# Optimization experiments

Measured on AMD Instinct MI355X. Metric: run time of the kernel, lower is better.

## Reference

```python
import jax, jax.numpy as jnp
import numpy as np

D_MODEL = 1024
NUM_HEADS = 16
HEAD_DIM = D_MODEL // NUM_HEADS


def setup_inputs() -> dict:
    key = jax.random.key(0)
    ks = jax.random.split(key, 6)
    B, S = 2, 2048
    w_scale = 1.0 / np.sqrt(D_MODEL)  # keep logits O(1) so the naive exp-softmax is stable
    return {
        "x": jax.random.normal(ks[0], (B, S, D_MODEL), dtype=jnp.float32),
        "y": jax.random.normal(ks[1], (B, S, D_MODEL), dtype=jnp.float32),
        "mask": jnp.zeros((S, S), dtype=jnp.float32),
        "Wq": jax.random.normal(ks[2], (D_MODEL, D_MODEL), dtype=jnp.float32) * w_scale,
        "Wk": jax.random.normal(ks[3], (D_MODEL, D_MODEL), dtype=jnp.float32) * w_scale,
        "Wv": jax.random.normal(ks[4], (D_MODEL, D_MODEL), dtype=jnp.float32) * w_scale,
        "Wo": jax.random.normal(ks[5], (D_MODEL, D_MODEL), dtype=jnp.float32) * w_scale,
    }


def _naive_softmax(s):
    # faithful to nirmalya_softmax: plain exp, sum + eps, no max subtraction
    p1 = jnp.exp(s)
    p2 = jnp.sum(p1, axis=-1, keepdims=True) + 1e-10
    return p1 / p2


def reference(x, y, mask, Wq, Wk, Wv, Wo):
    B, S, _ = x.shape
    # nn.Linear(bias=False): t @ W.T ; split heads -> [B, H, S, Dh]
    def split_heads(t):
        return t.reshape(B, S, NUM_HEADS, HEAD_DIM).transpose(0, 2, 1, 3)

    k = split_heads(x @ Wk.T)
    v = split_heads(x @ Wv.T)
    q = split_heads(y @ Wq.T)

    scores = jnp.einsum("bhqd,bhkd->bhqk", q, k) / np.sqrt(HEAD_DIM)
    scores = scores + mask  # [S,S] broadcasts over [B,H,S,S] (same math as permute-add-permute)
    attn = _naive_softmax(scores)
    out = jnp.einsum("bhqk,bhkd->bhqd", attn, v)  # [B,H,S,Dh]
    out = out.transpose(0, 2, 1, 3).reshape(B, S, D_MODEL)
    return out @ Wo.T
```

## Files before the change

kernel.cpp:

```cpp
#include <hip/hip_runtime.h>
#include <stdint.h>

typedef unsigned short u16;
typedef __attribute__((ext_vector_type(4))) float f32x4;
typedef __attribute__((ext_vector_type(2))) __bf16 bf16x2;
typedef __attribute__((ext_vector_type(8))) __bf16 bf16x8;
typedef __attribute__((ext_vector_type(4))) u16 u16x4;

#define AS1 __attribute__((address_space(1)))
#define AS3 __attribute__((address_space(3)))
#define GLOAD_LDS16(gp, lp) \
  __builtin_amdgcn_global_load_lds((const AS1 void*)(gp), (AS3 void*)(lp), 16, 0, 0)

__device__ __forceinline__ u16 f2bf(float f) {
  union { float f; unsigned u; } v; v.f = f;
  return (u16)((v.u + 0x7FFFu + ((v.u >> 16) & 1u)) >> 16);
}

__device__ __forceinline__ u16x4 pack4(float a, float b, float c, float d) {
#if __has_builtin(__builtin_amdgcn_cvt_pk_bf16_f32)
  union { struct { bf16x2 lo, hi; } p; u16x4 v; } u;
  u.p.lo = __builtin_amdgcn_cvt_pk_bf16_f32(a, b);
  u.p.hi = __builtin_amdgcn_cvt_pk_bf16_f32(c, d);
  return u.v;
#else
  u16x4 r; r.x = f2bf(a); r.y = f2bf(b); r.z = f2bf(c); r.w = f2bf(d); return r;
#endif
}

__global__ __launch_bounds__(256) void convert_all(
    const float* __restrict__ x, const float* __restrict__ y,
    const float* __restrict__ wq, const float* __restrict__ wk,
    const float* __restrict__ wv, const float* __restrict__ wo,
    u16* __restrict__ xb, u16* __restrict__ yb, u16* __restrict__ wqb,
    u16* __restrict__ wkb, u16* __restrict__ wvb, u16* __restrict__ wob) {
  size_t i = (size_t)blockIdx.x * 256 + threadIdx.x;
  const float* src; u16* dst; float scale = 1.0f; size_t off;
  if (i < (size_t)(1u << 20)) { src = x; dst = xb; off = i; }
  else if (i < (size_t)(2u << 20)) { src = y; dst = yb; off = i - (1u << 20); }
  else {
    size_t j = i - (size_t)(2u << 20);
    unsigned w = (unsigned)(j >> 18); off = j & ((1u << 18) - 1);
    if (w == 0)      { src = wq; dst = wqb; scale = 0.125f; }
    else if (w == 1) { src = wk; dst = wkb; }
    else if (w == 2) { src = wv; dst = wvb; }
    else             { src = wo; dst = wob; }
  }
  f32x4 v = ((const f32x4*)src)[off];
  ((u16x4*)dst)[off] = pack4(v.x * scale, v.y * scale, v.z * scale, v.w * scale);
}

__device__ __forceinline__ void gemm_core(
    const u16* __restrict__ A, const u16* __restrict__ Bt, int tm, int tn,
    u16* As, u16* Bs, f32x4 acc[4][4], int wave, int lane) {
  constexpr int K = 1024;
  const int l15 = lane & 15, quad = lane >> 4;
  const int wr = wave >> 1, wc = wave & 1;
  const int srow = lane >> 2;
  const int scol = ((lane & 3) ^ ((lane >> 3) & 3)) * 8;
  const u16* Ag = A + (size_t)(tm + wave * 32 + srow) * K + scol;
  const u16* Bg = Bt + (size_t)(tn + wave * 32 + srow) * K + scol;
  u16* Asl0 = &As[(wave * 2 + 0) * 512];
  u16* Asl1 = &As[(wave * 2 + 1) * 512];
  u16* Bsl0 = &Bs[(wave * 2 + 0) * 512];
  u16* Bsl1 = &Bs[(wave * 2 + 1) * 512];
  const int rc = (quad ^ ((l15 >> 1) & 3)) * 8;

  for (int k0 = 0; k0 < K; k0 += 32) {
    __syncthreads();
    GLOAD_LDS16(Ag + k0, Asl0);
    GLOAD_LDS16(Ag + 16 * K + k0, Asl1);
    GLOAD_LDS16(Bg + k0, Bsl0);
    GLOAD_LDS16(Bg + 16 * K + k0, Bsl1);
    __syncthreads();
    bf16x8 af[4], bfr[4];
#pragma unroll
    for (int mi = 0; mi < 4; ++mi)
      af[mi] = *(const bf16x8*)&As[(wr * 64 + mi * 16 + l15) * 32 + rc];
#pragma unroll
    for (int ni = 0; ni < 4; ++ni)
      bfr[ni] = *(const bf16x8*)&Bs[(wc * 64 + ni * 16 + l15) * 32 + rc];
#pragma unroll
    for (int mi = 0; mi < 4; ++mi)
#pragma unroll
      for (int ni = 0; ni < 4; ++ni)
        acc[mi][ni] = __builtin_amdgcn_mfma_f32_16x16x32_bf16(
            af[mi], bfr[ni], acc[mi][ni], 0, 0, 0);
  }
}

__global__ __launch_bounds__(256, 2) void qkv_gemm(
    const u16* __restrict__ xb, const u16* __restrict__ yb,
    const u16* __restrict__ wqb, const u16* __restrict__ wkb,
    const u16* __restrict__ wvb,
    u16* __restrict__ Qw, u16* __restrict__ Kw, u16* __restrict__ Vtw) {
  __shared__ __align__(16) u16 As[128 * 32];
  __shared__ __align__(16) u16 Bs[128 * 32];
  const int tid = threadIdx.x, wave = tid >> 6, lane = tid & 63;
  const int l15 = lane & 15, quad = lane >> 4;
  const int wr = wave >> 1, wc = wave & 1;
  const int z = blockIdx.z;
  const u16 *A, *Bt; int tm, tn;
  if (z == 0)      { A = yb;  Bt = wqb; tm = blockIdx.y * 128; tn = blockIdx.x * 128; }
  else if (z == 1) { A = xb;  Bt = wkb; tm = blockIdx.y * 128; tn = blockIdx.x * 128; }
  else             { A = wvb; Bt = xb;  tm = blockIdx.x * 128; tn = blockIdx.y * 128; }

  f32x4 acc[4][4] = {};
  gemm_core(A, Bt, tm, tn, As, Bs, acc, wave, lane);

#pragma unroll
  for (int mi = 0; mi < 4; ++mi) {
#pragma unroll
    for (int ni = 0; ni < 4; ++ni) {
#pragma unroll
      for (int r = 0; r < 4; ++r) {
        int gm = tm + wr * 64 + mi * 16 + quad * 4 + r;
        int gn = tn + wc * 64 + ni * 16 + l15;
        u16 val = f2bf(acc[mi][ni][r]);
        if (z == 2) {
          int h = gm >> 6, dh = gm & 63, b = gn >> 11, s = gn & 2047;
          Vtw[(((size_t)(b * 16 + h) * 64 + dh) << 11) + s] = val;
        } else {
          int b = gm >> 11, s = gm & 2047, h = gn >> 6, dh = gn & 63;
          u16* dst = (z == 0) ? Qw : Kw;
          dst[(((size_t)(b * 16 + h) * 2048 + s) << 6) + dh] = val;
        }
      }
    }
  }
}

__global__ __launch_bounds__(256, 2) void out_gemm(
    const u16* __restrict__ Ow, const u16* __restrict__ wob,
    float* __restrict__ C) {
  __shared__ __align__(16) u16 As[128 * 32];
  __shared__ __align__(16) u16 Bs[128 * 32];
  const int tid = threadIdx.x, wave = tid >> 6, lane = tid & 63;
  const int l15 = lane & 15, quad = lane >> 4;
  const int wr = wave >> 1, wc = wave & 1;
  const int tm = blockIdx.y * 128, tn = blockIdx.x * 128;

  f32x4 acc[4][4] = {};
  gemm_core(Ow, wob, tm, tn, As, Bs, acc, wave, lane);

#pragma unroll
  for (int mi = 0; mi < 4; ++mi)
#pragma unroll
    for (int ni = 0; ni < 4; ++ni)
#pragma unroll
      for (int r = 0; r < 4; ++r) {
        int gm = tm + wr * 64 + mi * 16 + quad * 4 + r;
        int gn = tn + wc * 64 + ni * 16 + l15;
        C[(size_t)gm * 1024 + gn] = acc[mi][ni][r];
      }
}

__global__ __launch_bounds__(256, 3) void attn_kernel(
    const u16* __restrict__ Qw, const u16* __restrict__ Kw,
    const u16* __restrict__ Vtw, const float* __restrict__ mask,
    u16* __restrict__ Ow) {
  constexpr int S = 2048;
  constexpr int PADK = 136;
  __shared__ __align__(16) u16 Ks[128 * 64];
  __shared__ __align__(16) u16 Vs[64 * 128];
  __shared__ __align__(16) u16 Ps[64 * PADK];
  const int tid = threadIdx.x;
  const int wave = tid >> 6, lane = tid & 63;
  const int l15 = lane & 15, quad = lane >> 4;
  const int qt = blockIdx.x, h = blockIdx.y, b = blockIdx.z;
  const size_t head = ((size_t)(b * 16 + h)) * S * 64;
  const int q_global = qt * 64 + wave * 16 + l15;

  bf16x8 qf[2];
#pragma unroll
  for (int kq = 0; kq < 2; ++kq)
    qf[kq] = *(const bf16x8*)&Qw[head + (size_t)q_global * 64 + kq * 32 + quad * 8];

  const __bf16 one_bf = (__bf16)1.0f;
  const bf16x8 ones = {one_bf, one_bf, one_bf, one_bf, one_bf, one_bf, one_bf, one_bf};

  f32x4 oa[4] = {};
  f32x4 den = {};

  const int k_r = lane >> 3;
  const int k_c = ((lane & 7) ^ ((lane >> 3) & 7)) * 8;
  const int v_r = lane >> 4;
  const int v_cbase = lane & 15;
  const float* mrow = mask + (size_t)q_global * S;

  for (int kt = 0; kt < S; kt += 128) {
    __syncthreads();
#pragma unroll
    for (int c = 0; c < 4; ++c) {
      int g = wave * 4 + c;
      GLOAD_LDS16(&Kw[head + (size_t)(kt + g * 8 + k_r) * 64 + k_c], &Ks[g * 512]);
    }
#pragma unroll
    for (int c = 0; c < 4; ++c) {
      int g = wave * 4 + c;
      int dh = g * 4 + v_r;
      int scb = (v_cbase ^ (dh & 15)) * 8;
      GLOAD_LDS16(&Vtw[head + (size_t)dh * S + kt + scb], &Vs[g * 512]);
    }
    f32x4 mv[8];
#pragma unroll
    for (int mk = 0; mk < 8; ++mk)
      mv[mk] = *(const f32x4*)&mrow[kt + mk * 16 + quad * 4];
    __syncthreads();

    f32x4 sa[8] = {};
#pragma unroll
    for (int kq = 0; kq < 2; ++kq) {
#pragma unroll
      for (int mk = 0; mk < 8; ++mk) {
        int row = mk * 16 + l15;
        bf16x8 ak = *(const bf16x8*)&Ks[row * 64 + (((kq * 4 + quad) ^ (l15 & 7)) * 8)];
        sa[mk] = __builtin_amdgcn_mfma_f32_16x16x32_bf16(ak, qf[kq], sa[mk], 0, 0, 0);
      }
    }

#pragma unroll
    for (int mk = 0; mk < 8; ++mk) {
      float p0 = __expf(sa[mk][0] + mv[mk][0]);
      float p1 = __expf(sa[mk][1] + mv[mk][1]);
      float p2 = __expf(sa[mk][2] + mv[mk][2]);
      float p3 = __expf(sa[mk][3] + mv[mk][3]);
      *(u16x4*)&Ps[(wave * 16 + l15) * PADK + mk * 16 + quad * 4] = pack4(p0, p1, p2, p3);
    }

#pragma unroll
    for (int kq2 = 0; kq2 < 4; ++kq2) {
      bf16x8 ap = *(const bf16x8*)&Ps[(wave * 16 + l15) * PADK + kq2 * 32 + quad * 8];
#pragma unroll
      for (int nv = 0; nv < 4; ++nv) {
        int row = nv * 16 + l15;
        bf16x8 bv = *(const bf16x8*)&Vs[row * 128 + (((kq2 * 4 + quad) ^ l15) * 8)];
        oa[nv] = __builtin_amdgcn_mfma_f32_16x16x32_bf16(ap, bv, oa[nv], 0, 0, 0);
      }
      den = __builtin_amdgcn_mfma_f32_16x16x32_bf16(ap, ones, den, 0, 0, 0);
    }
  }

#pragma unroll
  for (int nv = 0; nv < 4; ++nv) {
#pragma unroll
    for (int r = 0; r < 4; ++r) {
      int srow = qt * 64 + wave * 16 + quad * 4 + r;
      int dh = nv * 16 + l15;
      float val = oa[nv][r] / (den[r] + 1e-10f);
      Ow[((size_t)(b * S + srow) << 10) + h * 64 + dh] = f2bf(val);
    }
  }
}

extern "C" void kernel_launch(void* const* d_in, const int* in_sizes, int n_in,
                              void* d_out, int out_size, void* d_ws, size_t ws_size,
                              hipStream_t stream) {
  const float* x    = (const float*)d_in[0];
  const float* y    = (const float*)d_in[1];
  const float* mask = (const float*)d_in[2];
  const float* Wq   = (const float*)d_in[3];
  const float* Wk   = (const float*)d_in[4];
  const float* Wv   = (const float*)d_in[5];
  const float* Wo   = (const float*)d_in[6];
  char* ws = (char*)d_ws;
  const size_t MB = (size_t)1 << 20;
  u16* xb  = (u16*)(ws + 0  * MB);
  u16* yb  = (u16*)(ws + 8  * MB);
  u16* wqb = (u16*)(ws + 16 * MB);
  u16* wkb = (u16*)(ws + 18 * MB);
  u16* wvb = (u16*)(ws + 20 * MB);
  u16* wob = (u16*)(ws + 22 * MB);
  u16* Qw  = (u16*)(ws + 24 * MB);
  u16* Kw  = (u16*)(ws + 32 * MB);
  u16* Vtw = (u16*)(ws + 40 * MB);
  u16* Ow  = (u16*)(ws + 48 * MB);

  convert_all<<<12288, 256, 0, stream>>>(x, y, Wq, Wk, Wv, Wo,
                                         xb, yb, wqb, wkb, wvb, wob);
  qkv_gemm<<<dim3(8, 32, 3), 256, 0, stream>>>(xb, yb, wqb, wkb, wvb, Qw, Kw, Vtw);
  attn_kernel<<<dim3(32, 16, 2), 256, 0, stream>>>(Qw, Kw, Vtw, mask, Ow);
  out_gemm<<<dim3(8, 32), 256, 0, stream>>>(Ow, wob, (float*)d_out);
  (void)in_sizes; (void)n_in; (void)out_size; (void)ws_size;
}
```

Baseline: 267.5 us.

## Widen GEMM K-tile, double attention query rows, use exp2 and bf16 mask

The GEMM core now stages 64-wide K tiles with an 8-way XOR swizzle, which halves the number of barrier-separated iterations. The attention kernel gives each wave 32 query rows so every K/V fragment loaded from LDS feeds two MFMAs. Softmax switches to exp2, with log2e folded into Wq and the mask. The mask is converted to bf16 and stored temporarily in the output buffer, halving mask traffic, at the cost of rounding the mask and an extra conversion pass.

```diff
diff --git a/kernel.cpp b/kernel.cpp
--- a/kernel.cpp
+++ b/kernel.cpp
@@ -16,7 +16,16 @@
   union { float f; unsigned u; } v; v.f = f;
   return (u16)((v.u + 0x7FFFu + ((v.u >> 16) & 1u)) >> 16);
 }
-
+__device__ __forceinline__ float bf2f(u16 u) {
+  union { unsigned u; float f; } v; v.u = ((unsigned)u) << 16; return v.f;
+}
+__device__ __forceinline__ float fexp2(float x) {
+#if __has_builtin(__builtin_amdgcn_exp2f)
+  return __builtin_amdgcn_exp2f(x);
+#else
+  return exp2f(x);
+#endif
+}
 __device__ __forceinline__ u16x4 pack4(float a, float b, float c, float d) {
 #if __has_builtin(__builtin_amdgcn_cvt_pk_bf16_f32)
   union { struct { bf16x2 lo, hi; } p; u16x4 v; } u;
@@ -28,74 +37,81 @@
 #endif
 }
 
+#define LOG2E 1.44269504f
+
 __global__ __launch_bounds__(256) void convert_all(
     const float* __restrict__ x, const float* __restrict__ y,
     const float* __restrict__ wq, const float* __restrict__ wk,
     const float* __restrict__ wv, const float* __restrict__ wo,
+    const float* __restrict__ mask,
     u16* __restrict__ xb, u16* __restrict__ yb, u16* __restrict__ wqb,
-    u16* __restrict__ wkb, u16* __restrict__ wvb, u16* __restrict__ wob) {
+    u16* __restrict__ wkb, u16* __restrict__ wvb, u16* __restrict__ wob,
+    u16* __restrict__ maskb) {
   size_t i = (size_t)blockIdx.x * 256 + threadIdx.x;
   const float* src; u16* dst; float scale = 1.0f; size_t off;
   if (i < (size_t)(1u << 20)) { src = x; dst = xb; off = i; }
   else if (i < (size_t)(2u << 20)) { src = y; dst = yb; off = i - (1u << 20); }
-  else {
+  else if (i < (size_t)(3u << 20)) {
     size_t j = i - (size_t)(2u << 20);
     unsigned w = (unsigned)(j >> 18); off = j & ((1u << 18) - 1);
-    if (w == 0)      { src = wq; dst = wqb; scale = 0.125f; }
+    if (w == 0)      { src = wq; dst = wqb; scale = 0.125f * LOG2E; }
     else if (w == 1) { src = wk; dst = wkb; }
     else if (w == 2) { src = wv; dst = wvb; }
     else             { src = wo; dst = wob; }
-  }
+  } else { src = mask; dst = maskb; scale = LOG2E; off = i - (size_t)(3u << 20); }
   f32x4 v = ((const f32x4*)src)[off];
   ((u16x4*)dst)[off] = pack4(v.x * scale, v.y * scale, v.z * scale, v.w * scale);
 }
 
-__device__ __forceinline__ void gemm_core(
+__device__ __forceinline__ void gemm_core64(
     const u16* __restrict__ A, const u16* __restrict__ Bt, int tm, int tn,
     u16* As, u16* Bs, f32x4 acc[4][4], int wave, int lane) {
   constexpr int K = 1024;
   const int l15 = lane & 15, quad = lane >> 4;
   const int wr = wave >> 1, wc = wave & 1;
-  const int srow = lane >> 2;
-  const int scol = ((lane & 3) ^ ((lane >> 3) & 3)) * 8;
+  const int srow = lane >> 3;
+  const int scol = ((lane & 7) ^ (srow & 7)) * 8;
   const u16* Ag = A + (size_t)(tm + wave * 32 + srow) * K + scol;
   const u16* Bg = Bt + (size_t)(tn + wave * 32 + srow) * K + scol;
-  u16* Asl0 = &As[(wave * 2 + 0) * 512];
-  u16* Asl1 = &As[(wave * 2 + 1) * 512];
-  u16* Bsl0 = &Bs[(wave * 2 + 0) * 512];
-  u16* Bsl1 = &Bs[(wave * 2 + 1) * 512];
-  const int rc = (quad ^ ((l15 >> 1) & 3)) * 8;
-
-  for (int k0 = 0; k0 < K; k0 += 32) {
+  const int rsw = l15 & 7;
+
+  for (int k0 = 0; k0 < K; k0 += 64) {
     __syncthreads();
-    GLOAD_LDS16(Ag + k0, Asl0);
-    GLOAD_LDS16(Ag + 16 * K + k0, Asl1);
-    GLOAD_LDS16(Bg + k0, Bsl0);
-    GLOAD_LDS16(Bg + 16 * K + k0, Bsl1);
+#pragma unroll
+    for (int c = 0; c < 4; ++c)
+      GLOAD_LDS16(Ag + (size_t)c * 8 * K + k0, &As[(wave * 4 + c) * 512]);
+#pragma unroll
+    for (int c = 0; c < 4; ++c)
+      GLOAD_LDS16(Bg + (size_t)c * 8 * K + k0, &Bs[(wave * 4 + c) * 512]);
     __syncthreads();
-    bf16x8 af[4], bfr[4];
-#pragma unroll
-    for (int mi = 0; mi < 4; ++mi)
-      af[mi] = *(const bf16x8*)&As[(wr * 64 + mi * 16 + l15) * 32 + rc];
-#pragma unroll
-    for (int ni = 0; ni < 4; ++ni)
-      bfr[ni] = *(const bf16x8*)&Bs[(wc * 64 + ni * 16 + l15) * 32 + rc];
-#pragma unroll
-    for (int mi = 0; mi < 4; ++mi)
+#pragma unroll
+    for (int kq = 0; kq < 2; ++kq) {
+      bf16x8 af[4], bfr[4];
+#pragma unroll
+      for (int mi = 0; mi < 4; ++mi)
+        af[mi] = *(const bf16x8*)&As[(wr * 64 + mi * 16 + l15) * 64 +
+                                     ((kq * 4 + quad) ^ rsw) * 8];
 #pragma unroll
       for (int ni = 0; ni < 4; ++ni)
-        acc[mi][ni] = __builtin_amdgcn_mfma_f32_16x16x32_bf16(
-            af[mi], bfr[ni], acc[mi][ni], 0, 0, 0);
+        bfr[ni] = *(const bf16x8*)&Bs[(wc * 64 + ni * 16 + l15) * 64 +
+                                      ((kq * 4 + quad) ^ rsw) * 8];
+#pragma unroll
+      for (int mi = 0; mi < 4; ++mi)
+#pragma unroll
+        for (int ni = 0; ni < 4; ++ni)
+          acc[mi][ni] = __builtin_amdgcn_mfma_f32_16x16x32_bf16(
+              af[mi], bfr[ni], acc[mi][ni], 0, 0, 0);
+    }
   }
 }
 
-__global__ __launch_bounds__(256, 2) void qkv_gemm(
+__global__ __launch_bounds__(256, 3) void qkv_gemm(
     const u16* __restrict__ xb, const u16* __restrict__ yb,
     const u16* __restrict__ wqb, const u16* __restrict__ wkb,
     const u16* __restrict__ wvb,
     u16* __restrict__ Qw, u16* __restrict__ Kw, u16* __restrict__ Vtw) {
-  __shared__ __align__(16) u16 As[128 * 32];
-  __shared__ __align__(16) u16 Bs[128 * 32];
+  __shared__ __align__(16) u16 As[128 * 64];
+  __shared__ __align__(16) u16 Bs[128 * 64];
   const int tid = threadIdx.x, wave = tid >> 6, lane = tid & 63;
   const int l15 = lane & 15, quad = lane >> 4;
   const int wr = wave >> 1, wc = wave & 1;
@@ -106,7 +122,7 @@
   else             { A = wvb; Bt = xb;  tm = blockIdx.x * 128; tn = blockIdx.y * 128; }
 
   f32x4 acc[4][4] = {};
-  gemm_core(A, Bt, tm, tn, As, Bs, acc, wave, lane);
+  gemm_core64(A, Bt, tm, tn, As, Bs, acc, wave, lane);
 
 #pragma unroll
   for (int mi = 0; mi < 4; ++mi) {
@@ -130,18 +146,18 @@
   }
 }
 
-__global__ __launch_bounds__(256, 2) void out_gemm(
+__global__ __launch_bounds__(256, 3) void out_gemm(
     const u16* __restrict__ Ow, const u16* __restrict__ wob,
     float* __restrict__ C) {
-  __shared__ __align__(16) u16 As[128 * 32];
-  __shared__ __align__(16) u16 Bs[128 * 32];
+  __shared__ __align__(16) u16 As[128 * 64];
+  __shared__ __align__(16) u16 Bs[128 * 64];
   const int tid = threadIdx.x, wave = tid >> 6, lane = tid & 63;
   const int l15 = lane & 15, quad = lane >> 4;
   const int wr = wave >> 1, wc = wave & 1;
   const int tm = blockIdx.y * 128, tn = blockIdx.x * 128;
 
   f32x4 acc[4][4] = {};
-  gemm_core(Ow, wob, tm, tn, As, Bs, acc, wave, lane);
+  gemm_core64(Ow, wob, tm, tn, As, Bs, acc, wave, lane);
 
 #pragma unroll
   for (int mi = 0; mi < 4; ++mi)
@@ -155,100 +171,117 @@
       }
 }
 
-__global__ __launch_bounds__(256, 3) void attn_kernel(
+__global__ __launch_bounds__(256, 2) void attn_kernel(
     const u16* __restrict__ Qw, const u16* __restrict__ Kw,
-    const u16* __restrict__ Vtw, const float* __restrict__ mask,
+    const u16* __restrict__ Vtw, const u16* __restrict__ maskb,
     u16* __restrict__ Ow) {
   constexpr int S = 2048;
   constexpr int PADK = 136;
   __shared__ __align__(16) u16 Ks[128 * 64];
   __shared__ __align__(16) u16 Vs[64 * 128];
-  __shared__ __align__(16) u16 Ps[64 * PADK];
+  __shared__ __align__(16) u16 Ps[128 * PADK];
   const int tid = threadIdx.x;
   const int wave = tid >> 6, lane = tid & 63;
   const int l15 = lane & 15, quad = lane >> 4;
-  const int qt = blockIdx.x, h = blockIdx.y, b = blockIdx.z;
+  const int h = blockIdx.y, b = blockIdx.z;
   const size_t head = ((size_t)(b * 16 + h)) * S * 64;
-  const int q_global = qt * 64 + wave * 16 + l15;
-
-  bf16x8 qf[2];
-#pragma unroll
-  for (int kq = 0; kq < 2; ++kq)
-    qf[kq] = *(const bf16x8*)&Qw[head + (size_t)q_global * 64 + kq * 32 + quad * 8];
+  const int qbase = blockIdx.x * 128 + wave * 32;
+
+  bf16x8 qf[2][2];
+#pragma unroll
+  for (int q2 = 0; q2 < 2; ++q2)
+#pragma unroll
+    for (int kq = 0; kq < 2; ++kq)
+      qf[q2][kq] = *(const bf16x8*)&Qw[head +
+          (size_t)(qbase + q2 * 16 + l15) * 64 + kq * 32 + quad * 8];
 
   const __bf16 one_bf = (__bf16)1.0f;
   const bf16x8 ones = {one_bf, one_bf, one_bf, one_bf, one_bf, one_bf, one_bf, one_bf};
 
-  f32x4 oa[4] = {};
-  f32x4 den = {};
-
-  const int k_r = lane >> 3;
-  const int k_c = ((lane & 7) ^ ((lane >> 3) & 7)) * 8;
-  const int v_r = lane >> 4;
-  const int v_cbase = lane & 15;
-  const float* mrow = mask + (size_t)q_global * S;
+  f32x4 oa[2][4] = {};
+  f32x4 den[2] = {};
+
+  const int k_key = lane >> 3;
+  const int k_c = ((lane & 7) ^ (k_key & 7)) * 8;
+  const int v_dh = lane >> 4;
+  const int v_cl = lane & 15;
+  const u16* mrow[2] = { maskb + (size_t)(qbase + l15) * S,
+                         maskb + (size_t)(qbase + 16 + l15) * S };
 
   for (int kt = 0; kt < S; kt += 128) {
     __syncthreads();
 #pragma unroll
     for (int c = 0; c < 4; ++c) {
       int g = wave * 4 + c;
-      GLOAD_LDS16(&Kw[head + (size_t)(kt + g * 8 + k_r) * 64 + k_c], &Ks[g * 512]);
+      GLOAD_LDS16(&Kw[head + (size_t)(kt + g * 8 + k_key) * 64 + k_c], &Ks[g * 512]);
     }
 #pragma unroll
     for (int c = 0; c < 4; ++c) {
       int g = wave * 4 + c;
-      int dh = g * 4 + v_r;
-      int scb = (v_cbase ^ (dh & 15)) * 8;
-      GLOAD_LDS16(&Vtw[head + (size_t)dh * S + kt + scb], &Vs[g * 512]);
-    }
-    f32x4 mv[8];
-#pragma unroll
-    for (int mk = 0; mk < 8; ++mk)
-      mv[mk] = *(const f32x4*)&mrow[kt + mk * 16 + quad * 4];
+      int dh = g * 4 + v_dh;
+      GLOAD_LDS16(&Vtw[head + (size_t)dh * S + kt + ((v_cl ^ (dh & 15)) * 8)],
+                  &Vs[g * 512]);
+    }
+    u16x4 mq[2][8];
+#pragma unroll
+    for (int q2 = 0; q2 < 2; ++q2)
+#pragma unroll
+      for (int mk = 0; mk < 8; ++mk)
+        mq[q2][mk] = *(const u16x4*)&mrow[q2][kt + mk * 16 + quad * 4];
     __syncthreads();
 
-    f32x4 sa[8] = {};
+    f32x4 sa[2][8] = {};
 #pragma unroll
     for (int kq = 0; kq < 2; ++kq) {
 #pragma unroll
       for (int mk = 0; mk < 8; ++mk) {
-        int row = mk * 16 + l15;
-        bf16x8 ak = *(const bf16x8*)&Ks[row * 64 + (((kq * 4 + quad) ^ (l15 & 7)) * 8)];
-        sa[mk] = __builtin_amdgcn_mfma_f32_16x16x32_bf16(ak, qf[kq], sa[mk], 0, 0, 0);
-      }
-    }
-
-#pragma unroll
-    for (int mk = 0; mk < 8; ++mk) {
-      float p0 = __expf(sa[mk][0] + mv[mk][0]);
-      float p1 = __expf(sa[mk][1] + mv[mk][1]);
-      float p2 = __expf(sa[mk][2] + mv[mk][2]);
-      float p3 = __expf(sa[mk][3] + mv[mk][3]);
-      *(u16x4*)&Ps[(wave * 16 + l15) * PADK + mk * 16 + quad * 4] = pack4(p0, p1, p2, p3);
+        bf16x8 ak = *(const bf16x8*)&Ks[(mk * 16 + l15) * 64 +
+                                        ((kq * 4 + quad) ^ (l15 & 7)) * 8];
+        sa[0][mk] = __builtin_amdgcn_mfma_f32_16x16x32_bf16(ak, qf[0][kq], sa[0][mk], 0, 0, 0);
+        sa[1][mk] = __builtin_amdgcn_mfma_f32_16x16x32_bf16(ak, qf[1][kq], sa[1][mk], 0, 0, 0);
+      }
+    }
+
+#pragma unroll
+    for (int q2 = 0; q2 < 2; ++q2) {
+#pragma unroll
+      for (int mk = 0; mk < 8; ++mk) {
+        float p0 = fexp2(sa[q2][mk][0] + bf2f(mq[q2][mk].x));
+        float p1 = fexp2(sa[q2][mk][1] + bf2f(mq[q2][mk].y));
+        float p2 = fexp2(sa[q2][mk][2] + bf2f(mq[q2][mk].z));
+        float p3 = fexp2(sa[q2][mk][3] + bf2f(mq[q2][mk].w));
+        *(u16x4*)&Ps[(wave * 32 + q2 * 16 + l15) * PADK + mk * 16 + quad * 4] =
+            pack4(p0, p1, p2, p3);
+      }
     }
 
 #pragma unroll
     for (int kq2 = 0; kq2 < 4; ++kq2) {
-      bf16x8 ap = *(const bf16x8*)&Ps[(wave * 16 + l15) * PADK + kq2 * 32 + quad * 8];
+      bf16x8 ap0 = *(const bf16x8*)&Ps[(wave * 32 + l15) * PADK + kq2 * 32 + quad * 8];
+      bf16x8 ap1 = *(const bf16x8*)&Ps[(wave * 32 + 16 + l15) * PADK + kq2 * 32 + quad * 8];
 #pragma unroll
       for (int nv = 0; nv < 4; ++nv) {
-        int row = nv * 16 + l15;
-        bf16x8 bv = *(const bf16x8*)&Vs[row * 128 + (((kq2 * 4 + quad) ^ l15) * 8)];
-        oa[nv] = __builtin_amdgcn_mfma_f32_16x16x32_bf16(ap, bv, oa[nv], 0, 0, 0);
-      }
-      den = __builtin_amdgcn_mfma_f32_16x16x32_bf16(ap, ones, den, 0, 0, 0);
+        bf16x8 bv = *(const bf16x8*)&Vs[(nv * 16 + l15) * 128 +
+                                        ((kq2 * 4 + quad) ^ l15) * 8];
+        oa[0][nv] = __builtin_amdgcn_mfma_f32_16x16x32_bf16(ap0, bv, oa[0][nv], 0, 0, 0);
+        oa[1][nv] = __builtin_amdgcn_mfma_f32_16x16x32_bf16(ap1, bv, oa[1][nv], 0, 0, 0);
+      }
+      den[0] = __builtin_amdgcn_mfma_f32_16x16x32_bf16(ap0, ones, den[0], 0, 0, 0);
+      den[1] = __builtin_amdgcn_mfma_f32_16x16x32_bf16(ap1, ones, den[1], 0, 0, 0);
     }
   }
 
 #pragma unroll
-  for (int nv = 0; nv < 4; ++nv) {
-#pragma unroll
-    for (int r = 0; r < 4; ++r) {
-      int srow = qt * 64 + wave * 16 + quad * 4 + r;
-      int dh = nv * 16 + l15;
-      float val = oa[nv][r] / (den[r] + 1e-10f);
-      Ow[((size_t)(b * S + srow) << 10) + h * 64 + dh] = f2bf(val);
+  for (int q2 = 0; q2 < 2; ++q2) {
+#pragma unroll
+    for (int nv = 0; nv < 4; ++nv) {
+#pragma unroll
+      for (int r = 0; r < 4; ++r) {
+        int srow = qbase + q2 * 16 + quad * 4 + r;
+        int dh = nv * 16 + l15;
+        float val = oa[q2][nv][r] / (den[q2][r] + 1e-10f);
+        Ow[((size_t)(b * S + srow) << 10) + h * 64 + dh] = f2bf(val);
+      }
     }
   }
 }
@@ -275,11 +308,12 @@
   u16* Kw  = (u16*)(ws + 32 * MB);
   u16* Vtw = (u16*)(ws + 40 * MB);
   u16* Ow  = (u16*)(ws + 48 * MB);
-
-  convert_all<<<12288, 256, 0, stream>>>(x, y, Wq, Wk, Wv, Wo,
-                                         xb, yb, wqb, wkb, wvb, wob);
+  u16* maskb = (u16*)d_out;
+
+  convert_all<<<16384, 256, 0, stream>>>(x, y, Wq, Wk, Wv, Wo, mask,
+                                         xb, yb, wqb, wkb, wvb, wob, maskb);
   qkv_gemm<<<dim3(8, 32, 3), 256, 0, stream>>>(xb, yb, wqb, wkb, wvb, Qw, Kw, Vtw);
-  attn_kernel<<<dim3(32, 16, 2), 256, 0, stream>>>(Qw, Kw, Vtw, mask, Ow);
+  attn_kernel<<<dim3(16, 16, 2), 256, 0, stream>>>(Qw, Kw, Vtw, maskb, Ow);
   out_gemm<<<dim3(8, 32), 256, 0, stream>>>(Ow, wob, (float*)d_out);
   (void)in_sizes; (void)n_in; (void)out_size; (void)ws_size;
 }
```

Measured after the change: 246.3 us. 7.9% less time.
